# Kernel tuning notes

Measured on AMD Instinct MI355X. Metric: run time of the kernel, lower is better.

## Reference

```python
import jax, jax.numpy as jnp
import numpy as np

B, T, D, H = 4, 2048, 1024, 16
HD = D // H  # 64

def setup_inputs() -> dict:
    key = jax.random.key(0)
    ks = jax.random.split(key, 6)
    s = 0.02
    x = jax.random.normal(ks[0], (B, T, D), dtype=jnp.float32)
    # per-head projection weights, torch Linear layout [out=HD, in=D], stacked over heads
    Wq = jax.random.normal(ks[1], (H, HD, D), dtype=jnp.float32) * s
    Wk = jax.random.normal(ks[2], (H, HD, D), dtype=jnp.float32) * s
    Wv = jax.random.normal(ks[3], (H, HD, D), dtype=jnp.float32) * s
    Wo = jax.random.normal(ks[4], (D, D), dtype=jnp.float32) * s
    bo = jax.random.normal(ks[5], (D,), dtype=jnp.float32) * s
    return {"x": x, "Wq": Wq, "Wk": Wk, "Wv": Wv, "Wo": Wo, "bo": bo}

def reference(x, Wq, Wk, Wv, Wo, bo):
    # per-head projections (same math as per-head nn.Linear, vectorized over heads)
    Q = jnp.einsum('btd,hkd->bhtk', x, Wq)
    K = jnp.einsum('bsd,hkd->bhsk', x, Wk)
    V = jnp.einsum('bsd,hkd->bhsk', x, Wv)
    scale = 1.0 / jnp.sqrt(jnp.asarray(HD, x.dtype))
    logits = jnp.einsum('bhtk,bhsk->bhts', Q, K) * scale  # [B,H,T,S]
    w = jax.nn.softmax(logits, axis=-1)
    out = jnp.einsum('bhts,bhsk->bhtk', w, V)  # [B,H,T,HD]
    # concat heads in order -> [B,T,D]
    cat = jnp.transpose(out, (0, 2, 1, 3)).reshape(B, T, D)
    return cat @ Wo.T + bo
```

## Files before the change

kernel.cpp:

```cpp
#include <hip/hip_runtime.h>
#include <hip/hip_bf16.h>
#include <stdint.h>
#include <math.h>

typedef unsigned short u16;
typedef uint32_t u32;
typedef __bf16 bf16x8 __attribute__((ext_vector_type(8)));
typedef float f32x4 __attribute__((ext_vector_type(4)));
typedef float f32x16 __attribute__((ext_vector_type(16)));
typedef u16 u16x8 __attribute__((ext_vector_type(8)));
typedef u16 u16x4 __attribute__((ext_vector_type(4)));

#define B_ 4
#define T_ 2048
#define D_ 1024
#define H_ 16
#define HD_ 64
#define M_ (B_*T_)
#define LDA 72

__device__ __forceinline__ u16 f2bf(float f) {
    union { __bf16 h; u16 u; } c;
    c.h = (__bf16)f;
    return c.u;
}

__device__ __forceinline__ void gl16(const u16* g, u16* l) {
    __builtin_amdgcn_global_load_lds(
        (__attribute__((address_space(1))) void*)g,
        (__attribute__((address_space(3))) void*)l, 16, 0, 0);
}

__device__ __forceinline__ f32x4 mfma16(bf16x8 a, bf16x8 b, f32x4 c) {
    return __builtin_amdgcn_mfma_f32_16x16x32_bf16(a, b, c, 0, 0, 0);
}

__device__ __forceinline__ f32x16 mfma32(bf16x8 a, bf16x8 b, f32x16 c) {
    return __builtin_amdgcn_mfma_f32_32x32x16_bf16(a, b, c, 0, 0, 0);
}

__device__ __forceinline__ u32 cvtpk_bf16(float lo, float hi) {
    u32 r;
    asm("v_cvt_pk_bf16_f32 %0, %1, %2" : "=v"(r) : "v"(lo), "v"(hi));
    return r;
}

__device__ __forceinline__ float fexp2(float x) {
    return __builtin_amdgcn_exp2f(x);
}

__global__ __launch_bounds__(256) void precast(
    const float* __restrict__ x,  const float* __restrict__ wq,
    const float* __restrict__ wk, const float* __restrict__ wv,
    const float* __restrict__ wo,
    u16* __restrict__ xb, u16* __restrict__ wqb, u16* __restrict__ wkb,
    u16* __restrict__ wvb, u16* __restrict__ wob)
{
    const int which = blockIdx.y;
    const float* src; u16* dst; int n;
    switch (which) {
        case 0: src = x;  dst = xb;  n = M_ * D_;  break;
        case 1: src = wq; dst = wqb; n = D_ * D_;  break;
        case 2: src = wk; dst = wkb; n = D_ * D_;  break;
        case 3: src = wv; dst = wvb; n = D_ * D_;  break;
        default: src = wo; dst = wob; n = D_ * D_; break;
    }
    int i = (blockIdx.x * 256 + threadIdx.x) * 4;
    if (i >= n) return;
    float4 v = *(const float4*)&src[i];
    u16x4 p = { f2bf(v.x), f2bf(v.y), f2bf(v.z), f2bf(v.w) };
    *(u16x4*)&dst[i] = p;
}

__device__ __forceinline__ void gemm8_pipe(
    const u16* __restrict__ Xg, const u16* __restrict__ Wg,
    u16* As, u16* Bs,
    const int tid, const int wm, const int wn, const int l15, const int quad,
    f32x4 acc[4][4])
{
    const u16* asrc[4]; int adst[4];
#pragma unroll
    for (int i = 0; i < 4; ++i) {
        int c = tid + i * 512;
        int row = c >> 3, slot = c & 7;
        asrc[i] = Xg + (size_t)row * 1024 + (slot ^ (row & 7)) * 8;
        adst[i] = c * 8;
    }
    const u16* bsrc[2]; int bdst[2];
#pragma unroll
    for (int i = 0; i < 2; ++i) {
        int c = tid + i * 512;
        int row = c >> 3, slot = c & 7;
        bsrc[i] = Wg + (size_t)row * 1024 + (slot ^ (row & 7)) * 8;
        bdst[i] = c * 8;
    }
    const int sw = l15 & 7;
    const int so0 = (quad ^ sw) * 8;
    const int so1 = ((4 + quad) ^ sw) * 8;

#pragma unroll
    for (int tt = 0; tt < 2; ++tt) {
#pragma unroll
        for (int i = 0; i < 4; ++i) gl16(asrc[i] + tt * 64, As + tt * 16384 + adst[i]);
#pragma unroll
        for (int i = 0; i < 2; ++i) gl16(bsrc[i] + tt * 64, Bs + tt * 8192 + bdst[i]);
    }
    asm volatile("s_waitcnt vmcnt(6)" ::: "memory");
    __builtin_amdgcn_s_barrier();

#pragma unroll
    for (int t = 0; t < 16; ++t) {
        const u16* Ab = As + (t % 3) * 16384;
        const u16* Bb = Bs + (t % 3) * 8192;
        if (t + 2 < 16) {
            const int k2 = (t + 2) * 64;
            u16* An = As + ((t + 2) % 3) * 16384;
            u16* Bn = Bs + ((t + 2) % 3) * 8192;
#pragma unroll
            for (int i = 0; i < 4; ++i) gl16(asrc[i] + k2, An + adst[i]);
#pragma unroll
            for (int i = 0; i < 2; ++i) gl16(bsrc[i] + k2, Bn + bdst[i]);
        }
        __builtin_amdgcn_sched_barrier(0);
        bf16x8 af0[4], af1[4], bf0[4], bf1[4];
#pragma unroll
        for (int mf = 0; mf < 4; ++mf) {
            const int rr = (wm * 64 + mf * 16 + l15) * 64;
            af0[mf] = *(const bf16x8*)&Ab[rr + so0];
            af1[mf] = *(const bf16x8*)&Ab[rr + so1];
        }
#pragma unroll
        for (int nf = 0; nf < 4; ++nf) {
            const int rr = (wn * 64 + nf * 16 + l15) * 64;
            bf0[nf] = *(const bf16x8*)&Bb[rr + so0];
            bf1[nf] = *(const bf16x8*)&Bb[rr + so1];
        }
        __builtin_amdgcn_s_setprio(1);
#pragma unroll
        for (int mf = 0; mf < 4; ++mf)
#pragma unroll
            for (int nf = 0; nf < 4; ++nf)
                acc[mf][nf] = mfma16(af0[mf], bf0[nf], acc[mf][nf]);
#pragma unroll
        for (int mf = 0; mf < 4; ++mf)
#pragma unroll
            for (int nf = 0; nf < 4; ++nf)
                acc[mf][nf] = mfma16(af1[mf], bf1[nf], acc[mf][nf]);
        __builtin_amdgcn_s_setprio(0);
        __builtin_amdgcn_sched_barrier(0);
        if (t + 2 < 16)      asm volatile("s_waitcnt vmcnt(6)" ::: "memory");
        else if (t + 1 < 16) asm volatile("s_waitcnt vmcnt(0)" ::: "memory");
        __builtin_amdgcn_s_barrier();
    }
}

__global__ __launch_bounds__(512, 2) void qkv_gemm(
    const u16* __restrict__ Xb, const u16* __restrict__ W3,
    u16* __restrict__ Qo, u16* __restrict__ Ko, u16* __restrict__ Vo)
{
    __shared__ __attribute__((aligned(16))) u16 As[3 * 256 * 64];
    __shared__ __attribute__((aligned(16))) u16 Bs[3 * 128 * 64];

    const int wg = blockIdx.x + 24 * blockIdx.y;
    const int xcd = wg & 7, k = wg >> 3;
    const int by = xcd * 4 + (k / 24);
    const int bx = k % 24;
    const int n0 = bx * 128, m0 = by * 256;
    const u16* Xg = Xb + (size_t)m0 * 1024;
    const u16* Wg = W3 + (size_t)n0 * 1024;
    const int z = n0 >> 10;
    u16* Out = (z == 0) ? Qo : (z == 1) ? Ko : Vo;
    const float qs = (z == 0) ? 0.125f * 1.44269504088896340736f : 1.0f;

    const int tid = threadIdx.x;
    const int lane = tid & 63;
    const int wave = tid >> 6;
    const int wm = wave >> 1, wn = wave & 1;
    const int l15 = lane & 15, quad = lane >> 4;

    f32x4 acc[4][4];
#pragma unroll
    for (int i = 0; i < 4; ++i)
#pragma unroll
        for (int j = 0; j < 4; ++j) acc[i][j] = (f32x4){0.f, 0.f, 0.f, 0.f};

    gemm8_pipe(Xg, Wg, &As[0], &Bs[0], tid, wm, wn, l15, quad, acc);

#pragma unroll
    for (int mf = 0; mf < 4; ++mf)
#pragma unroll
        for (int nf = 0; nf < 4; ++nf)
#pragma unroll
            for (int r = 0; r < 4; ++r) {
                int row = m0 + wm * 64 + mf * 16 + quad * 4 + r;
                int colz = (n0 & 1023) + wn * 64 + nf * 16 + l15;
                int b = row >> 11;
                int t = row & 2047;
                int h = colz >> 6;
                int hd = colz & 63;
                Out[((b * H_ + h) * T_ + t) * HD_ + hd] = f2bf(acc[mf][nf][r] * qs);
            }
}

__global__ __launch_bounds__(512, 2) void out_gemm(
    const u16* __restrict__ Xb, const u16* __restrict__ W3,
    const float* __restrict__ bias, float* __restrict__ Out)
{
    __shared__ __attribute__((aligned(16))) u16 As[3 * 256 * 64];
    __shared__ __attribute__((aligned(16))) u16 Bs[3 * 128 * 64];

    const int wg = blockIdx.x + 8 * blockIdx.y;
    const int xcd = wg & 7, k = wg >> 3;
    const int by = xcd * 4 + (k / 8);
    const int bx = k & 7;
    const int n0 = bx * 128, m0 = by * 256;
    const u16* Xg = Xb + (size_t)m0 * 1024;
    const u16* Wg = W3 + (size_t)n0 * 1024;

    const int tid = threadIdx.x;
    const int lane = tid & 63;
    const int wave = tid >> 6;
    const int wm = wave >> 1, wn = wave & 1;
    const int l15 = lane & 15, quad = lane >> 4;

    f32x4 acc[4][4];
#pragma unroll
    for (int i = 0; i < 4; ++i)
#pragma unroll
        for (int j = 0; j < 4; ++j) acc[i][j] = (f32x4){0.f, 0.f, 0.f, 0.f};

    gemm8_pipe(Xg, Wg, &As[0], &Bs[0], tid, wm, wn, l15, quad, acc);

#pragma unroll
    for (int mf = 0; mf < 4; ++mf)
#pragma unroll
        for (int nf = 0; nf < 4; ++nf)
#pragma unroll
            for (int r = 0; r < 4; ++r) {
                int row = m0 + wm * 64 + mf * 16 + quad * 4 + r;
                int col = n0 + wn * 64 + nf * 16 + l15;
                Out[(size_t)row * 1024 + col] = acc[mf][nf][r] + bias[col];
            }
}

__global__ __launch_bounds__(256) void vtrans(
    const u16* __restrict__ Vin, u16* __restrict__ Vout)
{
    __shared__ __attribute__((aligned(16))) u16 Tt[64 * LDA];
    const int tid = threadIdx.x;
    const int t0 = blockIdx.x * 64;
    const size_t base = (size_t)blockIdx.y * T_ * HD_;

#pragma unroll
    for (int i = 0; i < 2; ++i) {
        int ch = tid + i * 256;
        int r = ch >> 3, c = (ch & 7) * 8;
        u16x8 v = *(const u16x8*)&Vin[base + (size_t)(t0 + r) * HD_ + c];
#pragma unroll
        for (int j = 0; j < 8; ++j) {
            int hd = c + j;
            int blk = (r >> 3) ^ ((hd >> 3) & 7);
            Tt[hd * LDA + blk * 8 + (r & 7)] = v[j];
        }
    }
    __syncthreads();
#pragma unroll
    for (int i = 0; i < 2; ++i) {
        int ch = tid + i * 256;
        int hd = ch >> 3, n = ch & 7;
        int k = (hd >> 3) & 7;
        u16x8 v = *(const u16x8*)&Tt[hd * LDA + ((n ^ k) * 8)];
        *(u16x8*)&Vout[base + (size_t)hd * T_ + t0 + n * 8] = v;
    }
}

__global__ __launch_bounds__(256, 2) void attn(
    const u16* __restrict__ Q, const u16* __restrict__ K,
    const u16* __restrict__ Vt_g, u16* __restrict__ O)
{
    __shared__ __attribute__((aligned(16))) u16 Ks[2 * 4096];
    __shared__ __attribute__((aligned(16))) u16 Vts[2 * 4096];
    __shared__ float lps[4 * 64];

    const int tid = threadIdx.x;
    const int lane = tid & 63, w = tid >> 6;
    const int l31 = lane & 31, hi = lane >> 5;

    const int wg = blockIdx.x + (T_ / 256) * (blockIdx.y + H_ * blockIdx.z);
    const int xcd = wg & 7, k8 = wg >> 3;
    const int bh = xcd + 8 * (k8 >> 3);
    const int xq = k8 & 7;
    const int b = bh >> 4, h = bh & 15;
    const int t0 = xq * 256 + w * 64;

    const size_t base = (size_t)bh * T_ * HD_;
    const u16* Kb = K + base;
    const u16* Vtb = Vt_g + base;
    const u16* Qb = Q + base + (size_t)t0 * HD_;

    const int ca = tid,        ra = ca >> 3,  sa = (ca & 7) ^ (ra & 7);
    const int cb2 = tid + 256, rb = cb2 >> 3, sb = (cb2 & 7) ^ (rb & 7);
    const u16* kpa = Kb  + (size_t)ra * 64 + sa * 8;
    const u16* kpb = Kb  + (size_t)rb * 64 + sb * 8;
    const u16* vpa = Vtb + (size_t)ra * T_ + sa * 8;
    const u16* vpb = Vtb + (size_t)rb * T_ + sb * 8;

    int foff[2][4];
#pragma unroll
    for (int nt = 0; nt < 2; ++nt) {
        const int row = nt * 32 + l31;
#pragma unroll
        for (int kb = 0; kb < 4; ++kb)
            foff[nt][kb] = row * 64 + (((kb * 2 + hi) ^ (row & 7)) * 8);
    }

    bf16x8 qf[2][4];
#pragma unroll
    for (int qt = 0; qt < 2; ++qt)
#pragma unroll
        for (int kb = 0; kb < 4; ++kb)
            qf[qt][kb] = *(const bf16x8*)&Qb[(qt * 32 + l31) * 64 + kb * 16 + hi * 8];

    f32x16 zacc;
#pragma unroll
    for (int i = 0; i < 16; ++i) zacc[i] = 0.f;
    f32x16 oacc[2][2];
#pragma unroll
    for (int qt = 0; qt < 2; ++qt)
#pragma unroll
        for (int cb = 0; cb < 2; ++cb) oacc[qt][cb] = zacc;
    float lp[2] = {0.f, 0.f};

    gl16(kpa, &Ks[ca * 8]);
    gl16(kpb, &Ks[cb2 * 8]);
    gl16(vpa, &Vts[ca * 8]);
    gl16(vpb, &Vts[cb2 * 8]);
    asm volatile("s_waitcnt vmcnt(0)" ::: "memory");
    __syncthreads();

    int buf = 0;
    for (int s0 = 0; s0 < T_; s0 += 64) {
        if (s0 + 64 < T_) {
            const int nb = buf ^ 1;
            const size_t ko = (size_t)(s0 + 64) * 64;
            const size_t vo = (size_t)(s0 + 64);
            gl16(kpa + ko, &Ks[nb * 4096 + ca * 8]);
            gl16(kpb + ko, &Ks[nb * 4096 + cb2 * 8]);
            gl16(vpa + vo, &Vts[nb * 4096 + ca * 8]);
            gl16(vpb + vo, &Vts[nb * 4096 + cb2 * 8]);
        }
        const u16* Kc = &Ks[buf * 4096];
        const u16* Vc = &Vts[buf * 4096];

        bf16x8 pa[2][4];
#pragma unroll
        for (int nt = 0; nt < 2; ++nt) {
            bf16x8 kf[4];
#pragma unroll
            for (int kb = 0; kb < 4; ++kb)
                kf[kb] = *(const bf16x8*)&Kc[foff[nt][kb]];
#pragma unroll
            for (int qt = 0; qt < 2; ++qt) {
                __builtin_amdgcn_s_setprio(1);
                f32x16 sacc = mfma32(kf[0], qf[qt][0], zacc);
                sacc = mfma32(kf[1], qf[qt][1], sacc);
                sacc = mfma32(kf[2], qf[qt][2], sacc);
                sacc = mfma32(kf[3], qf[qt][3], sacc);
                __builtin_amdgcn_s_setprio(0);
                float p[16];
#pragma unroll
                for (int r = 0; r < 16; ++r) p[r] = fexp2(sacc[r]);
                float s01 = (p[0] + p[1]) + (p[2] + p[3]);
                float s23 = (p[4] + p[5]) + (p[6] + p[7]);
                float s45 = (p[8] + p[9]) + (p[10] + p[11]);
                float s67 = (p[12] + p[13]) + (p[14] + p[15]);
                lp[qt] += (s01 + s23) + (s45 + s67);
#pragma unroll
                for (int c = 0; c < 2; ++c) {
                    const int g = c * 8;
                    u32 a0 = cvtpk_bf16(p[g + 0], p[g + 1]);
                    u32 a1 = cvtpk_bf16(p[g + 2], p[g + 3]);
                    u32 b0 = cvtpk_bf16(p[g + 4], p[g + 5]);
                    u32 b1 = cvtpk_bf16(p[g + 6], p[g + 7]);
                    asm("v_permlane32_swap_b32 %0, %1" : "+v"(a0), "+v"(b0));
                    asm("v_permlane32_swap_b32 %0, %1" : "+v"(a1), "+v"(b1));
                    union { u32 wq[4]; bf16x8 v; } uu;
                    uu.wq[0] = a0; uu.wq[1] = a1; uu.wq[2] = b0; uu.wq[3] = b1;
                    pa[qt][nt * 2 + c] = uu.v;
                }
            }
        }
        __builtin_amdgcn_s_setprio(1);
#pragma unroll
        for (int cb = 0; cb < 2; ++cb)
#pragma unroll
            for (int kb = 0; kb < 4; ++kb) {
                bf16x8 vf = *(const bf16x8*)&Vc[foff[cb][kb]];
                oacc[0][cb] = mfma32(pa[0][kb], vf, oacc[0][cb]);
                oacc[1][cb] = mfma32(pa[1][kb], vf, oacc[1][cb]);
            }
        __builtin_amdgcn_s_setprio(0);
        asm volatile("s_waitcnt vmcnt(0)" ::: "memory");
        __syncthreads();
        buf ^= 1;
    }

#pragma unroll
    for (int qt = 0; qt < 2; ++qt) {
        lp[qt] += __shfl_xor(lp[qt], 32);
        lps[w * 64 + qt * 32 + l31] = lp[qt];
    }
    asm volatile("s_waitcnt lgkmcnt(0)" ::: "memory");

#pragma unroll
    for (int qt = 0; qt < 2; ++qt)
#pragma unroll
        for (int r = 0; r < 16; ++r) {
            const int trow = (r & 3) + 8 * (r >> 2) + 4 * hi;
            const float dn = 1.f / lps[w * 64 + qt * 32 + trow];
            const int t = t0 + qt * 32 + trow;
#pragma unroll
            for (int cb = 0; cb < 2; ++cb) {
                const int col = h * 64 + cb * 32 + l31;
                O[((size_t)b * T_ + t) * D_ + col] = f2bf(oacc[qt][cb][r] * dn);
            }
        }
}

extern "C" void kernel_launch(void* const* d_in, const int* in_sizes, int n_in,
                              void* d_out, int out_size, void* d_ws, size_t ws_size,
                              hipStream_t stream) {
    const float* x  = (const float*)d_in[0];
    const float* Wq = (const float*)d_in[1];
    const float* Wk = (const float*)d_in[2];
    const float* Wv = (const float*)d_in[3];
    const float* Wo = (const float*)d_in[4];
    const float* bo = (const float*)d_in[5];
    float* out = (float*)d_out;

    const size_t n_qkv = (size_t)B_ * H_ * T_ * HD_;
    const size_t n_w   = (size_t)D_ * D_;
    u16* Qw  = (u16*)d_ws;
    u16* Kw  = Qw + n_qkv;
    u16* Vw  = Kw + n_qkv;
    u16* Vtw = Vw + n_qkv;
    u16* Xb  = Vtw;
    u16* Wqb = Vtw + n_qkv;
    u16* Wkb = Wqb + n_w;
    u16* Wvb = Wkb + n_w;
    u16* Wob = Wvb + n_w;
    u16* Ow  = Vw;

    dim3 gc(8192, 5);
    precast<<<gc, 256, 0, stream>>>(x, Wq, Wk, Wv, Wo, Xb, Wqb, Wkb, Wvb, Wob);

    dim3 g1(3072 / 128, M_ / 256);
    qkv_gemm<<<g1, 512, 0, stream>>>(Xb, Wqb, Qw, Kw, Vw);

    dim3 gt(T_ / 64, B_ * H_);
    vtrans<<<gt, 256, 0, stream>>>(Vw, Vtw);

    dim3 g2(T_ / 256, H_, B_);
    attn<<<g2, 256, 0, stream>>>(Qw, Kw, Vtw, Ow);

    dim3 g3(1024 / 128, M_ / 256);
    out_gemm<<<g3, 512, 0, stream>>>(Ow, Wob, bo, out);
}
```

Measured before the change: 268.5 us.

## Fuse V transpose into QKV GEMM epilogue, reschedule attention softmax, flatten precast grid

The QKV GEMM now writes V directly in transposed [B,H,HD,T] layout using 4-element vector stores, so the separate vtrans kernel and its extra V round trip are dropped. The attention inner loop computes all four QK^T tiles first, preloads V fragments, then alternates softmax packing with PV MFMAs so exp work can overlap matrix work. The precast kernel uses a flat 1-D grid with no idle blocks, replacing the 5-row grid where most weight blocks exited early. Risks include uncoalesced transposed stores from the GEMM and higher register pressure in attention.

```diff
diff --git a/kernel.cpp b/kernel.cpp
--- a/kernel.cpp
+++ b/kernel.cpp
@@ -17,7 +17,6 @@
 #define H_ 16
 #define HD_ 64
 #define M_ (B_*T_)
-#define LDA 72
 
 __device__ __forceinline__ u16 f2bf(float f) {
     union { __bf16 h; u16 u; } c;
@@ -47,6 +46,37 @@
 
 __device__ __forceinline__ float fexp2(float x) {
     return __builtin_amdgcn_exp2f(x);
+}
+
+__device__ __forceinline__ void softmax_pack(
+    const f32x16& sacc, float& lp, bf16x8& paA, bf16x8& paB)
+{
+    float p[16];
+#pragma unroll
+    for (int r = 0; r < 16; ++r) p[r] = fexp2(sacc[r]);
+    float s01 = (p[0] + p[1]) + (p[2] + p[3]);
+    float s23 = (p[4] + p[5]) + (p[6] + p[7]);
+    float s45 = (p[8] + p[9]) + (p[10] + p[11]);
+    float s67 = (p[12] + p[13]) + (p[14] + p[15]);
+    lp += (s01 + s23) + (s45 + s67);
+    u32 a0 = cvtpk_bf16(p[0], p[1]);
+    u32 a1 = cvtpk_bf16(p[2], p[3]);
+    u32 b0 = cvtpk_bf16(p[4], p[5]);
+    u32 b1 = cvtpk_bf16(p[6], p[7]);
+    asm("v_permlane32_swap_b32 %0, %1" : "+v"(a0), "+v"(b0));
+    asm("v_permlane32_swap_b32 %0, %1" : "+v"(a1), "+v"(b1));
+    union { u32 wq[4]; bf16x8 v; } uA;
+    uA.wq[0] = a0; uA.wq[1] = a1; uA.wq[2] = b0; uA.wq[3] = b1;
+    paA = uA.v;
+    u32 c0 = cvtpk_bf16(p[8], p[9]);
+    u32 c1 = cvtpk_bf16(p[10], p[11]);
+    u32 d0 = cvtpk_bf16(p[12], p[13]);
+    u32 d1 = cvtpk_bf16(p[14], p[15]);
+    asm("v_permlane32_swap_b32 %0, %1" : "+v"(c0), "+v"(d0));
+    asm("v_permlane32_swap_b32 %0, %1" : "+v"(c1), "+v"(d1));
+    union { u32 wq[4]; bf16x8 v; } uB;
+    uB.wq[0] = c0; uB.wq[1] = c1; uB.wq[2] = d0; uB.wq[3] = d1;
+    paB = uB.v;
 }
 
 __global__ __launch_bounds__(256) void precast(
@@ -56,20 +86,24 @@
     u16* __restrict__ xb, u16* __restrict__ wqb, u16* __restrict__ wkb,
     u16* __restrict__ wvb, u16* __restrict__ wob)
 {
-    const int which = blockIdx.y;
-    const float* src; u16* dst; int n;
-    switch (which) {
-        case 0: src = x;  dst = xb;  n = M_ * D_;  break;
-        case 1: src = wq; dst = wqb; n = D_ * D_;  break;
-        case 2: src = wk; dst = wkb; n = D_ * D_;  break;
-        case 3: src = wv; dst = wvb; n = D_ * D_;  break;
-        default: src = wo; dst = wob; n = D_ * D_; break;
-    }
-    int i = (blockIdx.x * 256 + threadIdx.x) * 4;
-    if (i >= n) return;
-    float4 v = *(const float4*)&src[i];
+    const int i = (blockIdx.x * 256 + threadIdx.x) * 4;
+    const int nx = M_ * D_;
+    const float* src; u16* dst; int off;
+    if (i < nx) { src = x; dst = xb; off = i; }
+    else {
+        int j = i - nx;
+        int w = j >> 20;
+        off = j & ((1 << 20) - 1);
+        switch (w) {
+            case 0: src = wq; dst = wqb; break;
+            case 1: src = wk; dst = wkb; break;
+            case 2: src = wv; dst = wvb; break;
+            default: src = wo; dst = wob; break;
+        }
+    }
+    float4 v = *(const float4*)&src[off];
     u16x4 p = { f2bf(v.x), f2bf(v.y), f2bf(v.z), f2bf(v.w) };
-    *(u16x4*)&dst[i] = p;
+    *(u16x4*)&dst[off] = p;
 }
 
 __device__ __forceinline__ void gemm8_pipe(
@@ -156,7 +190,7 @@
 
 __global__ __launch_bounds__(512, 2) void qkv_gemm(
     const u16* __restrict__ Xb, const u16* __restrict__ W3,
-    u16* __restrict__ Qo, u16* __restrict__ Ko, u16* __restrict__ Vo)
+    u16* __restrict__ Qo, u16* __restrict__ Ko, u16* __restrict__ Vt)
 {
     __shared__ __attribute__((aligned(16))) u16 As[3 * 256 * 64];
     __shared__ __attribute__((aligned(16))) u16 Bs[3 * 128 * 64];
@@ -169,7 +203,6 @@
     const u16* Xg = Xb + (size_t)m0 * 1024;
     const u16* Wg = W3 + (size_t)n0 * 1024;
     const int z = n0 >> 10;
-    u16* Out = (z == 0) ? Qo : (z == 1) ? Ko : Vo;
     const float qs = (z == 0) ? 0.125f * 1.44269504088896340736f : 1.0f;
 
     const int tid = threadIdx.x;
@@ -186,20 +219,38 @@
 
     gemm8_pipe(Xg, Wg, &As[0], &Bs[0], tid, wm, wn, l15, quad, acc);
 
-#pragma unroll
-    for (int mf = 0; mf < 4; ++mf)
-#pragma unroll
-        for (int nf = 0; nf < 4; ++nf)
-#pragma unroll
-            for (int r = 0; r < 4; ++r) {
-                int row = m0 + wm * 64 + mf * 16 + quad * 4 + r;
+    if (z == 2) {
+#pragma unroll
+        for (int mf = 0; mf < 4; ++mf)
+#pragma unroll
+            for (int nf = 0; nf < 4; ++nf) {
+                int row0 = m0 + wm * 64 + mf * 16 + quad * 4;
                 int colz = (n0 & 1023) + wn * 64 + nf * 16 + l15;
-                int b = row >> 11;
-                int t = row & 2047;
+                int b = row0 >> 11;
+                int t = row0 & 2047;
                 int h = colz >> 6;
                 int hd = colz & 63;
-                Out[((b * H_ + h) * T_ + t) * HD_ + hd] = f2bf(acc[mf][nf][r] * qs);
+                u16x4 pv = { f2bf(acc[mf][nf][0]), f2bf(acc[mf][nf][1]),
+                             f2bf(acc[mf][nf][2]), f2bf(acc[mf][nf][3]) };
+                *(u16x4*)&Vt[(((size_t)(b * H_ + h) * HD_ + hd)) * T_ + t] = pv;
             }
+    } else {
+        u16* Out = (z == 0) ? Qo : Ko;
+#pragma unroll
+        for (int mf = 0; mf < 4; ++mf)
+#pragma unroll
+            for (int nf = 0; nf < 4; ++nf)
+#pragma unroll
+                for (int r = 0; r < 4; ++r) {
+                    int row = m0 + wm * 64 + mf * 16 + quad * 4 + r;
+                    int colz = (n0 & 1023) + wn * 64 + nf * 16 + l15;
+                    int b = row >> 11;
+                    int t = row & 2047;
+                    int h = colz >> 6;
+                    int hd = colz & 63;
+                    Out[((b * H_ + h) * T_ + t) * HD_ + hd] = f2bf(acc[mf][nf][r] * qs);
+                }
+    }
 }
 
 __global__ __launch_bounds__(512, 2) void out_gemm(
@@ -241,37 +292,6 @@
                 int col = n0 + wn * 64 + nf * 16 + l15;
                 Out[(size_t)row * 1024 + col] = acc[mf][nf][r] + bias[col];
             }
-}
-
-__global__ __launch_bounds__(256) void vtrans(
-    const u16* __restrict__ Vin, u16* __restrict__ Vout)
-{
-    __shared__ __attribute__((aligned(16))) u16 Tt[64 * LDA];
-    const int tid = threadIdx.x;
-    const int t0 = blockIdx.x * 64;
-    const size_t base = (size_t)blockIdx.y * T_ * HD_;
-
-#pragma unroll
-    for (int i = 0; i < 2; ++i) {
-        int ch = tid + i * 256;
-        int r = ch >> 3, c = (ch & 7) * 8;
-        u16x8 v = *(const u16x8*)&Vin[base + (size_t)(t0 + r) * HD_ + c];
-#pragma unroll
-        for (int j = 0; j < 8; ++j) {
-            int hd = c + j;
-            int blk = (r >> 3) ^ ((hd >> 3) & 7);
-            Tt[hd * LDA + blk * 8 + (r & 7)] = v[j];
-        }
-    }
-    __syncthreads();
-#pragma unroll
-    for (int i = 0; i < 2; ++i) {
-        int ch = tid + i * 256;
-        int hd = ch >> 3, n = ch & 7;
-        int k = (hd >> 3) & 7;
-        u16x8 v = *(const u16x8*)&Tt[hd * LDA + ((n ^ k) * 8)];
-        *(u16x8*)&Vout[base + (size_t)hd * T_ + t0 + n * 8] = v;
-    }
 }
 
 __global__ __launch_bounds__(256, 2) void attn(
@@ -352,54 +372,60 @@
         const u16* Kc = &Ks[buf * 4096];
         const u16* Vc = &Vts[buf * 4096];
 
-        bf16x8 pa[2][4];
-#pragma unroll
-        for (int nt = 0; nt < 2; ++nt) {
-            bf16x8 kf[4];
+        bf16x8 kf0[4], kf1[4];
+#pragma unroll
+        for (int kb = 0; kb < 4; ++kb) {
+            kf0[kb] = *(const bf16x8*)&Kc[foff[0][kb]];
+            kf1[kb] = *(const bf16x8*)&Kc[foff[1][kb]];
+        }
+        __builtin_amdgcn_s_setprio(1);
+        f32x16 s00 = mfma32(kf0[0], qf[0][0], zacc);
+        f32x16 s01 = mfma32(kf0[0], qf[1][0], zacc);
+        f32x16 s10 = mfma32(kf1[0], qf[0][0], zacc);
+        f32x16 s11 = mfma32(kf1[0], qf[1][0], zacc);
+#pragma unroll
+        for (int kb = 1; kb < 4; ++kb) {
+            s00 = mfma32(kf0[kb], qf[0][kb], s00);
+            s01 = mfma32(kf0[kb], qf[1][kb], s01);
+            s10 = mfma32(kf1[kb], qf[0][kb], s10);
+            s11 = mfma32(kf1[kb], qf[1][kb], s11);
+        }
+        __builtin_amdgcn_s_setprio(0);
+
+        bf16x8 vf[2][4];
+#pragma unroll
+        for (int cb = 0; cb < 2; ++cb)
 #pragma unroll
             for (int kb = 0; kb < 4; ++kb)
-                kf[kb] = *(const bf16x8*)&Kc[foff[nt][kb]];
-#pragma unroll
-            for (int qt = 0; qt < 2; ++qt) {
-                __builtin_amdgcn_s_setprio(1);
-                f32x16 sacc = mfma32(kf[0], qf[qt][0], zacc);
-                sacc = mfma32(kf[1], qf[qt][1], sacc);
-                sacc = mfma32(kf[2], qf[qt][2], sacc);
-                sacc = mfma32(kf[3], qf[qt][3], sacc);
-                __builtin_amdgcn_s_setprio(0);
-                float p[16];
-#pragma unroll
-                for (int r = 0; r < 16; ++r) p[r] = fexp2(sacc[r]);
-                float s01 = (p[0] + p[1]) + (p[2] + p[3]);
-                float s23 = (p[4] + p[5]) + (p[6] + p[7]);
-                float s45 = (p[8] + p[9]) + (p[10] + p[11]);
-                float s67 = (p[12] + p[13]) + (p[14] + p[15]);
-                lp[qt] += (s01 + s23) + (s45 + s67);
-#pragma unroll
-                for (int c = 0; c < 2; ++c) {
-                    const int g = c * 8;
-                    u32 a0 = cvtpk_bf16(p[g + 0], p[g + 1]);
-                    u32 a1 = cvtpk_bf16(p[g + 2], p[g + 3]);
-                    u32 b0 = cvtpk_bf16(p[g + 4], p[g + 5]);
-                    u32 b1 = cvtpk_bf16(p[g + 6], p[g + 7]);
-                    asm("v_permlane32_swap_b32 %0, %1" : "+v"(a0), "+v"(b0));
-                    asm("v_permlane32_swap_b32 %0, %1" : "+v"(a1), "+v"(b1));
-                    union { u32 wq[4]; bf16x8 v; } uu;
-                    uu.wq[0] = a0; uu.wq[1] = a1; uu.wq[2] = b0; uu.wq[3] = b1;
-                    pa[qt][nt * 2 + c] = uu.v;
-                }
-            }
-        }
+                vf[cb][kb] = *(const bf16x8*)&Vc[foff[cb][kb]];
+
+        bf16x8 pa0[2][2], pa1[2][2];
+        softmax_pack(s00, lp[0], pa0[0][0], pa0[0][1]);
+        softmax_pack(s01, lp[1], pa0[1][0], pa0[1][1]);
+
         __builtin_amdgcn_s_setprio(1);
 #pragma unroll
         for (int cb = 0; cb < 2; ++cb)
 #pragma unroll
-            for (int kb = 0; kb < 4; ++kb) {
-                bf16x8 vf = *(const bf16x8*)&Vc[foff[cb][kb]];
-                oacc[0][cb] = mfma32(pa[0][kb], vf, oacc[0][cb]);
-                oacc[1][cb] = mfma32(pa[1][kb], vf, oacc[1][cb]);
+            for (int kb = 0; kb < 2; ++kb) {
+                oacc[0][cb] = mfma32(pa0[0][kb], vf[cb][kb], oacc[0][cb]);
+                oacc[1][cb] = mfma32(pa0[1][kb], vf[cb][kb], oacc[1][cb]);
             }
         __builtin_amdgcn_s_setprio(0);
+
+        softmax_pack(s10, lp[0], pa1[0][0], pa1[0][1]);
+        softmax_pack(s11, lp[1], pa1[1][0], pa1[1][1]);
+
+        __builtin_amdgcn_s_setprio(1);
+#pragma unroll
+        for (int cb = 0; cb < 2; ++cb)
+#pragma unroll
+            for (int kb = 0; kb < 2; ++kb) {
+                oacc[0][cb] = mfma32(pa1[0][kb], vf[cb][kb + 2], oacc[0][cb]);
+                oacc[1][cb] = mfma32(pa1[1][kb], vf[cb][kb + 2], oacc[1][cb]);
+            }
+        __builtin_amdgcn_s_setprio(0);
+
         asm volatile("s_waitcnt vmcnt(0)" ::: "memory");
         __syncthreads();
         buf ^= 1;
@@ -440,25 +466,22 @@
 
     const size_t n_qkv = (size_t)B_ * H_ * T_ * HD_;
     const size_t n_w   = (size_t)D_ * D_;
-    u16* Qw  = (u16*)d_ws;
-    u16* Kw  = Qw + n_qkv;
-    u16* Vw  = Kw + n_qkv;
-    u16* Vtw = Vw + n_qkv;
-    u16* Xb  = Vtw;
-    u16* Wqb = Vtw + n_qkv;
-    u16* Wkb = Wqb + n_w;
-    u16* Wvb = Wkb + n_w;
-    u16* Wob = Wvb + n_w;
-    u16* Ow  = Vw;
-
-    dim3 gc(8192, 5);
+    u16* Qw   = (u16*)d_ws;
+    u16* Kw   = Qw + n_qkv;
+    u16* Vtw  = Kw + n_qkv;
+    u16* XbOw = Vtw + n_qkv;
+    u16* Xb   = XbOw;
+    u16* Ow   = XbOw;
+    u16* Wqb  = XbOw + n_qkv;
+    u16* Wkb  = Wqb + n_w;
+    u16* Wvb  = Wkb + n_w;
+    u16* Wob  = Wvb + n_w;
+
+    dim3 gc(12288);
     precast<<<gc, 256, 0, stream>>>(x, Wq, Wk, Wv, Wo, Xb, Wqb, Wkb, Wvb, Wob);
 
     dim3 g1(3072 / 128, M_ / 256);
-    qkv_gemm<<<g1, 512, 0, stream>>>(Xb, Wqb, Qw, Kw, Vw);
-
-    dim3 gt(T_ / 64, B_ * H_);
-    vtrans<<<gt, 256, 0, stream>>>(Vw, Vtw);
+    qkv_gemm<<<g1, 512, 0, stream>>>(Xb, Wqb, Qw, Kw, Vtw);
 
     dim3 g2(T_ / 256, H_, B_);
     attn<<<g2, 256, 0, stream>>>(Qw, Kw, Vtw, Ow);
```

After: 263.7 us. Within noise of the previous version (-1.8%).
